# Kernel optimization log

Measured on AMD Instinct MI355X. Metric: run time of the kernel, lower is better.

Reference implementation:

```python
import jax, jax.numpy as jnp
import numpy as np


def _h(s):
    # Step function: 0 where s > 0, else 1 (zero gradient everywhere).
    return jnp.where(s > 0, 0.0, 1.0).astype(s.dtype)


def setup_inputs() -> dict:
    key = jax.random.key(0)
    k1, k2, k3 = jax.random.split(key, 3)
    B, T = 4096, 2048
    x = jax.random.normal(k1, (B, T, 1), dtype=jnp.float32)
    out_prev = jax.random.normal(k2, (B, 1, 1), dtype=jnp.float32)
    lstm_outs = jax.random.normal(k3, (B, T, 4), dtype=jnp.float32)
    return {"x": x, "out_prev": out_prev, "lstm_outs": lstm_outs}


def reference(x, out_prev, lstm_outs):
    # x: [B, T, 1], out_prev: [B, 1, 1] (only first step used), lstm_outs: [B, T, 4]
    xT = jnp.swapaxes(x, 0, 1)          # [T, B, 1]
    wT = jnp.swapaxes(lstm_outs, 0, 1)  # [T, B, 4]

    def step(prev, inputs):
        # prev: [B, 1]
        xt, wt = inputs                  # [B, 1], [B, 4]
        m_lo = wt[:, 0:1]
        m_up = wt[:, 1:2]
        c_lo = wt[:, 2:3]
        c_up = wt[:, 3:4]
        # h() arguments use detached weights in the original (grad is zero through
        # the step function anyway); stop_gradient kept for faithfulness.
        m_lo_d = jax.lax.stop_gradient(m_lo)
        m_up_d = jax.lax.stop_gradient(m_up)
        c_lo_d = jax.lax.stop_gradient(c_lo)
        c_up_d = jax.lax.stop_gradient(c_up)
        f1 = _h((m_lo_d * xt + m_lo_d * c_lo_d - prev) / m_lo_d)
        f2 = _h((prev - m_up_d * xt - m_up_d * c_up_d) / m_up_d)
        out = (m_lo * xt * f1 + m_lo * c_lo * f1
               + m_up * xt * f2 + m_up * c_up * f2
               + prev * (1.0 - f1) * (1.0 - f2))
        return out, out

    init = out_prev[:, 0, :]             # [B, 1]
    _, outs = jax.lax.scan(step, init, (xT, wT))  # outs: [T, B, 1]
    custom_output = jnp.swapaxes(outs, 0, 1)      # [B, T, 1]
    # Original also returns (lstm_outs, 0, 0, 0) passthrough; main output is below.
    return custom_output
```

## Files before the change

### kernel.cpp

```cpp
#include <hip/hip_runtime.h>


#define C 64
#define NCH 32
#define NTB 3
#define NOB 4
#define TS 65
#define XS 68

#define CFENCE() asm volatile("" ::: "memory")

__global__ __launch_bounds__(192) void pc_scan(
    const float* __restrict__ x, const float* __restrict__ p0,
    const float4* __restrict__ lstm4, float* __restrict__ out,
    int B, int T) {
#pragma clang fp contract(off)
  __shared__ float4 tileA[NTB][16 * TS];
  __shared__ float4 tileB[NTB][16 * TS];
  __shared__ float xt[16 * XS];
  __shared__ float ostg[NOB][16 * XS];
  __shared__ int stagedw[2][NCH];
  __shared__ int scanned;

  const int tid = threadIdx.x;
  const int b0 = blockIdx.x * 16;
  const float4* x4 = reinterpret_cast<const float4*>(x);
  float4* out4 = reinterpret_cast<float4*>(out);

  for (int i = tid; i < 2 * NCH; i += 192) ((int*)stagedw)[i] = 0;
  if (tid == 0) scanned = 0;
  __syncthreads();

  if (tid >= 64) {
    const int q = tid - 64;
    const int pj = (q >> 3) & 15;
    const int pk = q & 7;
    const int w = (tid >> 6) - 1;
    const bool lead = (q & 63) == 0;

    float4 L00, L01, L02, L03, L04, L05, L06, L07;
    float4 L10, L11, L12, L13, L14, L15, L16, L17;
    float4 X00, X01, X10, X11;

#define ISSUE(S, CH)                                                    \
  {                                                                     \
    size_t rb = (size_t)(b0 + pj) * T + (size_t)(CH) * C;               \
    const float4* lp = lstm4 + rb + pk;                                 \
    L##S##0 = lp[0];  L##S##1 = lp[8];  L##S##2 = lp[16];               \
    L##S##3 = lp[24]; L##S##4 = lp[32]; L##S##5 = lp[40];               \
    L##S##6 = lp[48]; L##S##7 = lp[56];                                 \
    X##S##0 = x4[(rb >> 2) + 2 * pk];                                   \
    X##S##1 = x4[(rb >> 2) + 2 * pk + 1];                               \
  }

#define STAGE_ELT(LV, SS, BUF)                                          \
  {                                                                     \
    float4 wv = LV;                       \
    float xv = xt[pj * XS + (SS)];                                      \
    float a1 = wv.x * xv, a2 = wv.x * wv.z;                             \
    float L1v = a1 + a2;                                                \
    unsigned s1m = __float_as_uint(wv.x) & 0x80000000u;                 \
    float L1f = __uint_as_float(__float_as_uint(L1v) ^ s1m);            \
    float a3 = wv.y * xv, a4 = wv.y * wv.w;                             \
    unsigned f2m = (__float_as_uint(wv.y) & 0x80000000u) ^ 0x80000000u; \
    float a3f = __uint_as_float(__float_as_uint(a3) ^ f2m);             \
    float a4f = __uint_as_float(__float_as_uint(a4) ^ f2m);             \
    float V01 = a3 + a4;                                                \
    float V11 = (L1v + a3) + a4;                                        \
    tileA[BUF][pj * TS + (SS)] =                                        \
        make_float4(__uint_as_float(s1m), L1f, __uint_as_float(f2m), a3f); \
    tileB[BUF][pj * TS + (SS)] = make_float4(a4f, V11, V01, L1v);       \
  }

#define STAGE(S, BUF)                                                   \
  {                                                                     \
    *(float4*)&xt[pj * XS + 8 * pk] = X##S##0;                          \
    *(float4*)&xt[pj * XS + 8 * pk + 4] = X##S##1;                      \
    STAGE_ELT(L##S##0, pk,      BUF)                                    \
    STAGE_ELT(L##S##1, pk + 8,  BUF)                                    \
    STAGE_ELT(L##S##2, pk + 16, BUF)                                    \
    STAGE_ELT(L##S##3, pk + 24, BUF)                                    \
    STAGE_ELT(L##S##4, pk + 32, BUF)                                    \
    STAGE_ELT(L##S##5, pk + 40, BUF)                                    \
    STAGE_ELT(L##S##6, pk + 48, BUF)                                    \
    STAGE_ELT(L##S##7, pk + 56, BUF)                                    \
  }

#define FLUSH(CP, OB)                                                   \
  {                                                                     \
    float4 v0 = *(const float4*)&ostg[OB][pj * XS + 8 * pk];            \
    float4 v1 = *(const float4*)&ostg[OB][pj * XS + 8 * pk + 4];        \
    size_t ob = ((size_t)(b0 + pj) * T + (size_t)(CP) * C) >> 2;        \
    out4[ob + 2 * pk] = v0;                                             \
    out4[ob + 2 * pk + 1] = v1;                                         \
  }

#define PWAIT(TGT)                                                      \
  while (*(volatile int*)&scanned < (TGT)) __builtin_amdgcn_s_sleep(1); \
  CFENCE();

    ISSUE(0, 0)
    ISSUE(1, 1)

    for (int k = 0; k < NCH; k += 2) {
      PWAIT(k - 2)
      STAGE(0, k % NTB)
      CFENCE();
      if (lead) *(volatile int*)&stagedw[w][k] = 1;
      if (k + 2 < NCH) ISSUE(0, k + 2)
      if (k >= 3) FLUSH(k - 3, (k - 3) % NOB)
      PWAIT(k - 1)
      STAGE(1, (k + 1) % NTB)
      CFENCE();
      if (lead) *(volatile int*)&stagedw[w][k + 1] = 1;
      if (k + 3 < NCH) ISSUE(1, k + 3)
      if (k >= 2) FLUSH(k - 2, (k - 2) % NOB)
    }
    for (int j = NCH - 3; j < NCH; ++j) {
      PWAIT(j + 1)
      FLUSH(j, j % NOB)
    }
  } else {
    float p = (tid < 16) ? p0[b0 + tid] : 0.0f;

#define RSTEP(I, OVC)                                                   \
  {                                                                     \
    float4 A = rA##I;                                                   \
    float4 Bv = rB##I;                                                  \
    if (g < 7) {                                                        \
      rA##I = ta[8 * g + 8 + I];                                        \
      rB##I = tb[8 * g + 8 + I];                                        \
    }                                                                   \
    unsigned pu = __float_as_uint(p);                                   \
    float pf = __uint_as_float(pu ^ __float_as_uint(A.x));              \
    bool c1 = pf >= A.y;                                                \
    float pp = __uint_as_float(pu ^ __float_as_uint(A.z));              \
    float qv = pp - A.w;                                                \
    bool c2 = qv >= Bv.x;                                               \
    float i1 = c1 ? Bv.y : Bv.z;                                        \
    float i2 = c1 ? Bv.w : p;                                           \
    p = c2 ? i1 : i2;                                                   \
    OVC = p;                                                            \
  }

    for (int c = 0; c < NCH; ++c) {
      for (;;) {
        int a = *(volatile int*)&stagedw[0][c];
        int b = *(volatile int*)&stagedw[1][c];
        if (a + b == 2) break;
        __builtin_amdgcn_s_sleep(1);
      }
      CFENCE();
      if (tid < 16) {
        const float4* ta = &tileA[c % NTB][tid * TS];
        const float4* tb = &tileB[c % NTB][tid * TS];
        float* orow = &ostg[c % NOB][tid * XS];
        float4 rA0 = ta[0], rA1 = ta[1], rA2 = ta[2], rA3 = ta[3];
        float4 rA4 = ta[4], rA5 = ta[5], rA6 = ta[6], rA7 = ta[7];
        float4 rB0 = tb[0], rB1 = tb[1], rB2 = tb[2], rB3 = tb[3];
        float4 rB4 = tb[4], rB5 = tb[5], rB6 = tb[6], rB7 = tb[7];
#pragma unroll
        for (int g = 0; g < 8; ++g) {
          float4 ov0, ov1;
          RSTEP(0, ov0.x) RSTEP(1, ov0.y) RSTEP(2, ov0.z) RSTEP(3, ov0.w)
          RSTEP(4, ov1.x) RSTEP(5, ov1.y) RSTEP(6, ov1.z) RSTEP(7, ov1.w)
          *(float4*)&orow[8 * g] = ov0;
          *(float4*)&orow[8 * g + 4] = ov1;
        }
      }
      CFENCE();
      if (tid == 0) *(volatile int*)&scanned = c + 1;
    }
  }
}

extern "C" void kernel_launch(void* const* d_in, const int* in_sizes, int n_in,
                              void* d_out, int out_size, void* d_ws, size_t ws_size,
                              hipStream_t stream) {
  const float* x = (const float*)d_in[0];
  const float* op = (const float*)d_in[1];
  const float4* lstm = (const float4*)d_in[2];
  int B = in_sizes[1];
  int T = in_sizes[0] / B;
  hipLaunchKernelGGL(pc_scan, dim3(B / 16), dim3(192), 0, stream,
                     x, op, lstm, (float*)d_out, B, T);
}
```

Before: 231.3 us.

## Replace warp-specialized LDS pipeline with per-thread fused scan with register prefetch

Drops the producer/consumer design, where two wavefronts staged precomputed terms in shared memory for a 16-lane scan wavefront, and replaces it with a simple kernel. Each of 4 active lanes per 64-thread block scans one row directly from global memory. It keeps a triple-buffered register prefetch two groups ahead and writes outputs straight to global. This removes LDS traffic and spin-wait synchronization but leaves only 4 of 64 lanes active, and each lane makes strided, uncoalesced per-thread loads. The loop count of 256 groups is hardcoded, which assumes T=2048.

```diff
diff --git a/kernel.cpp b/kernel.cpp
--- a/kernel.cpp
+++ b/kernel.cpp
@@ -1,62 +1,40 @@
 #include <hip/hip_runtime.h>
 
 
-#define C 64
-#define NCH 32
-#define NTB 3
-#define NOB 4
-#define TS 65
-#define XS 68
+#define NG 256
+#define ROWS 4
 
-#define CFENCE() asm volatile("" ::: "memory")
-
-__global__ __launch_bounds__(192) void pc_scan(
+__global__ __launch_bounds__(64) void fused_scan(
     const float* __restrict__ x, const float* __restrict__ p0,
     const float4* __restrict__ lstm4, float* __restrict__ out,
     int B, int T) {
 #pragma clang fp contract(off)
-  __shared__ float4 tileA[NTB][16 * TS];
-  __shared__ float4 tileB[NTB][16 * TS];
-  __shared__ float xt[16 * XS];
-  __shared__ float ostg[NOB][16 * XS];
-  __shared__ int stagedw[2][NCH];
-  __shared__ int scanned;
+  const int lane = threadIdx.x;
+  if (lane >= ROWS) return;
+  const size_t row = (size_t)blockIdx.x * ROWS + lane;
+  const size_t rbase = row * (size_t)T;
+  const float4* lp = lstm4 + rbase;
+  const float4* xp = reinterpret_cast<const float4*>(x + rbase);
+  float4* op = reinterpret_cast<float4*>(out + rbase);
+  float p = p0[row];
 
-  const int tid = threadIdx.x;
-  const int b0 = blockIdx.x * 16;
-  const float4* x4 = reinterpret_cast<const float4*>(x);
-  float4* out4 = reinterpret_cast<float4*>(out);
+  float4 L0E, L1E, L2E, L3E, L4E, L5E, L6E, L7E, X0E, X1E;
+  float4 L0O, L1O, L2O, L3O, L4O, L5O, L6O, L7O, X0O, X1O;
+  float4 L0F, L1F, L2F, L3F, L4F, L5F, L6F, L7F, X0F, X1F;
 
-  for (int i = tid; i < 2 * NCH; i += 192) ((int*)stagedw)[i] = 0;
-  if (tid == 0) scanned = 0;
-  __syncthreads();
-
-  if (tid >= 64) {
-    const int q = tid - 64;
-    const int pj = (q >> 3) & 15;
-    const int pk = q & 7;
-    const int w = (tid >> 6) - 1;
-    const bool lead = (q & 63) == 0;
-
-    float4 L00, L01, L02, L03, L04, L05, L06, L07;
-    float4 L10, L11, L12, L13, L14, L15, L16, L17;
-    float4 X00, X01, X10, X11;
-
-#define ISSUE(S, CH)                                                    \
+#define LOADG(S, G)                                                     \
   {                                                                     \
-    size_t rb = (size_t)(b0 + pj) * T + (size_t)(CH) * C;               \
-    const float4* lp = lstm4 + rb + pk;                                 \
-    L##S##0 = lp[0];  L##S##1 = lp[8];  L##S##2 = lp[16];               \
-    L##S##3 = lp[24]; L##S##4 = lp[32]; L##S##5 = lp[40];               \
-    L##S##6 = lp[48]; L##S##7 = lp[56];                                 \
-    X##S##0 = x4[(rb >> 2) + 2 * pk];                                   \
-    X##S##1 = x4[(rb >> 2) + 2 * pk + 1];                               \
+    const float4* lb = lp + 8 * (G);                                    \
+    L0##S = lb[0]; L1##S = lb[1]; L2##S = lb[2]; L3##S = lb[3];         \
+    L4##S = lb[4]; L5##S = lb[5]; L6##S = lb[6]; L7##S = lb[7];         \
+    X0##S = xp[2 * (G)];                                                \
+    X1##S = xp[2 * (G) + 1];                                            \
   }
 
-#define STAGE_ELT(LV, SS, BUF)                                          \
+#define STEP(WV, XV, OV)                                                \
   {                                                                     \
-    float4 wv = LV;                       \
-    float xv = xt[pj * XS + (SS)];                                      \
+    float4 wv = WV;                       \
+    float xv = XV;                                                      \
     float a1 = wv.x * xv, a2 = wv.x * wv.z;                             \
     float L1v = a1 + a2;                                                \
     unsigned s1m = __float_as_uint(wv.x) & 0x80000000u;                 \
@@ -67,111 +45,45 @@
     float a4f = __uint_as_float(__float_as_uint(a4) ^ f2m);             \
     float V01 = a3 + a4;                                                \
     float V11 = (L1v + a3) + a4;                                        \
-    tileA[BUF][pj * TS + (SS)] =                                        \
-        make_float4(__uint_as_float(s1m), L1f, __uint_as_float(f2m), a3f); \
-    tileB[BUF][pj * TS + (SS)] = make_float4(a4f, V11, V01, L1v);       \
+    unsigned pu = __float_as_uint(p);                                   \
+    float pf = __uint_as_float(pu ^ s1m);                               \
+    bool c1 = pf >= L1f;                                                \
+    float pp = __uint_as_float(pu ^ f2m);                               \
+    float qv = pp - a3f;                                                \
+    bool c2 = qv >= a4f;                                                \
+    float i1 = c1 ? V11 : V01;                                          \
+    float i2 = c1 ? L1v : p;                                            \
+    p = c2 ? i1 : i2;                                                   \
+    OV = p;                                                             \
   }
 
-#define STAGE(S, BUF)                                                   \
+#define BODY(CUR, PRE, G)                                               \
   {                                                                     \
-    *(float4*)&xt[pj * XS + 8 * pk] = X##S##0;                          \
-    *(float4*)&xt[pj * XS + 8 * pk + 4] = X##S##1;                      \
-    STAGE_ELT(L##S##0, pk,      BUF)                                    \
-    STAGE_ELT(L##S##1, pk + 8,  BUF)                                    \
-    STAGE_ELT(L##S##2, pk + 16, BUF)                                    \
-    STAGE_ELT(L##S##3, pk + 24, BUF)                                    \
-    STAGE_ELT(L##S##4, pk + 32, BUF)                                    \
-    STAGE_ELT(L##S##5, pk + 40, BUF)                                    \
-    STAGE_ELT(L##S##6, pk + 48, BUF)                                    \
-    STAGE_ELT(L##S##7, pk + 56, BUF)                                    \
+    int pg = (G) + 2;                                                   \
+    pg = (pg > NG - 1) ? (NG - 1) : pg;                                 \
+    LOADG(PRE, pg)                                                      \
+    float4 ov0, ov1;                                                    \
+    STEP(L0##CUR, X0##CUR.x, ov0.x)                                     \
+    STEP(L1##CUR, X0##CUR.y, ov0.y)                                     \
+    STEP(L2##CUR, X0##CUR.z, ov0.z)                                     \
+    STEP(L3##CUR, X0##CUR.w, ov0.w)                                     \
+    STEP(L4##CUR, X1##CUR.x, ov1.x)                                     \
+    STEP(L5##CUR, X1##CUR.y, ov1.y)                                     \
+    STEP(L6##CUR, X1##CUR.z, ov1.z)                                     \
+    STEP(L7##CUR, X1##CUR.w, ov1.w)                                     \
+    op[2 * (G)] = ov0;                                                  \
+    op[2 * (G) + 1] = ov1;                                              \
   }
 
-#define FLUSH(CP, OB)                                                   \
-  {                                                                     \
-    float4 v0 = *(const float4*)&ostg[OB][pj * XS + 8 * pk];            \
-    float4 v1 = *(const float4*)&ostg[OB][pj * XS + 8 * pk + 4];        \
-    size_t ob = ((size_t)(b0 + pj) * T + (size_t)(CP) * C) >> 2;        \
-    out4[ob + 2 * pk] = v0;                                             \
-    out4[ob + 2 * pk + 1] = v1;                                         \
+  LOADG(E, 0)
+  LOADG(O, 1)
+  for (int it = 0; it < 85; ++it) {
+    int g = 3 * it;
+    BODY(E, F, g)
+    BODY(O, E, g + 1)
+    BODY(F, O, g + 2)
   }
-
-#define PWAIT(TGT)                                                      \
-  while (*(volatile int*)&scanned < (TGT)) __builtin_amdgcn_s_sleep(1); \
-  CFENCE();
-
-    ISSUE(0, 0)
-    ISSUE(1, 1)
-
-    for (int k = 0; k < NCH; k += 2) {
-      PWAIT(k - 2)
-      STAGE(0, k % NTB)
-      CFENCE();
-      if (lead) *(volatile int*)&stagedw[w][k] = 1;
-      if (k + 2 < NCH) ISSUE(0, k + 2)
-      if (k >= 3) FLUSH(k - 3, (k - 3) % NOB)
-      PWAIT(k - 1)
-      STAGE(1, (k + 1) % NTB)
-      CFENCE();
-      if (lead) *(volatile int*)&stagedw[w][k + 1] = 1;
-      if (k + 3 < NCH) ISSUE(1, k + 3)
-      if (k >= 2) FLUSH(k - 2, (k - 2) % NOB)
-    }
-    for (int j = NCH - 3; j < NCH; ++j) {
-      PWAIT(j + 1)
-      FLUSH(j, j % NOB)
-    }
-  } else {
-    float p = (tid < 16) ? p0[b0 + tid] : 0.0f;
-
-#define RSTEP(I, OVC)                                                   \
-  {                                                                     \
-    float4 A = rA##I;                                                   \
-    float4 Bv = rB##I;                                                  \
-    if (g < 7) {                                                        \
-      rA##I = ta[8 * g + 8 + I];                                        \
-      rB##I = tb[8 * g + 8 + I];                                        \
-    }                                                                   \
-    unsigned pu = __float_as_uint(p);                                   \
-    float pf = __uint_as_float(pu ^ __float_as_uint(A.x));              \
-    bool c1 = pf >= A.y;                                                \
-    float pp = __uint_as_float(pu ^ __float_as_uint(A.z));              \
-    float qv = pp - A.w;                                                \
-    bool c2 = qv >= Bv.x;                                               \
-    float i1 = c1 ? Bv.y : Bv.z;                                        \
-    float i2 = c1 ? Bv.w : p;                                           \
-    p = c2 ? i1 : i2;                                                   \
-    OVC = p;                                                            \
-  }
-
-    for (int c = 0; c < NCH; ++c) {
-      for (;;) {
-        int a = *(volatile int*)&stagedw[0][c];
-        int b = *(volatile int*)&stagedw[1][c];
-        if (a + b == 2) break;
-        __builtin_amdgcn_s_sleep(1);
-      }
-      CFENCE();
-      if (tid < 16) {
-        const float4* ta = &tileA[c % NTB][tid * TS];
-        const float4* tb = &tileB[c % NTB][tid * TS];
-        float* orow = &ostg[c % NOB][tid * XS];
-        float4 rA0 = ta[0], rA1 = ta[1], rA2 = ta[2], rA3 = ta[3];
-        float4 rA4 = ta[4], rA5 = ta[5], rA6 = ta[6], rA7 = ta[7];
-        float4 rB0 = tb[0], rB1 = tb[1], rB2 = tb[2], rB3 = tb[3];
-        float4 rB4 = tb[4], rB5 = tb[5], rB6 = tb[6], rB7 = tb[7];
-#pragma unroll
-        for (int g = 0; g < 8; ++g) {
-          float4 ov0, ov1;
-          RSTEP(0, ov0.x) RSTEP(1, ov0.y) RSTEP(2, ov0.z) RSTEP(3, ov0.w)
-          RSTEP(4, ov1.x) RSTEP(5, ov1.y) RSTEP(6, ov1.z) RSTEP(7, ov1.w)
-          *(float4*)&orow[8 * g] = ov0;
-          *(float4*)&orow[8 * g + 4] = ov1;
-        }
-      }
-      CFENCE();
-      if (tid == 0) *(volatile int*)&scanned = c + 1;
-    }
-  }
+  BODY(E, F, NG - 1)
 }
 
 extern "C" void kernel_launch(void* const* d_in, const int* in_sizes, int n_in,
@@ -182,6 +94,6 @@
   const float4* lstm = (const float4*)d_in[2];
   int B = in_sizes[1];
   int T = in_sizes[0] / B;
-  hipLaunchKernelGGL(pc_scan, dim3(B / 16), dim3(192), 0, stream,
+  hipLaunchKernelGGL(fused_scan, dim3(B / ROWS), dim3(64), 0, stream,
                      x, op, lstm, (float*)d_out, B, T);
 }
```

New measurement: 547.9 us. +136.9%, slower.
